# Performance work log

Measured on AMD Instinct MI355X. Metric: run time of the kernel, lower is better.

## Reference

```python
import jax, jax.numpy as jnp
import numpy as np

B, K, M, MN = 256, 32, 64, 256
E, H, Q = 128, 128, 128
NE, NR, NNODES = 100000, 500, 256  # entities, relations, max_nodes


def setup_inputs() -> dict:
    key = jax.random.key(0)
    ks = jax.random.split(key, 24)
    f = lambda k, s: jax.random.normal(k, s, jnp.float32) * 0.05
    inp = {}
    inp['start_entities'] = jax.random.randint(ks[0], (B,), 0, NE)
    inp['aims'] = jax.random.randint(ks[1], (B, K), 0, NE)
    inp['node_pos'] = jnp.broadcast_to(jnp.arange(1, K + 1, dtype=jnp.int32), (B, K))
    inp['neighbor_nodes'] = jax.random.randint(ks[2], (B, K, M), 0, NNODES)
    inp['neighbor_relations'] = jax.random.randint(ks[3], (B, K, M), 0, NR)
    inp['neighbors_num'] = jax.random.randint(ks[4], (B, K), 0, M + 1)
    inp['currents'] = jax.random.randint(ks[5], (B,), 0, NNODES)
    inp['candidate_nodes'] = jax.random.randint(ks[6], (B, MN), 0, NNODES)
    inp['candidate_entities'] = jax.random.randint(ks[7], (B, MN), 0, NE)
    inp['candidate_relations'] = jax.random.randint(ks[8], (B, MN), 0, NR)
    inp['candidate_masks'] = jax.random.randint(ks[9], (B, MN), 0, 2).astype(bool)
    inp['entity_emb'] = f(ks[10], (NE, E))
    inp['relation_emb'] = f(ks[11], (NR, E))
    inp['hidden_W'] = f(ks[12], (H, E)); inp['hidden_b'] = f(ks[13], (H,))
    inp['pass_W'] = f(ks[14], (H, H + E)); inp['pass_b'] = f(ks[15], (H,))
    inp['nexthop_W'] = f(ks[16], (H, H + Q)); inp['nexthop_b'] = f(ks[17], (H,))
    inp['candidate_W'] = f(ks[18], (H, H + 2 * E)); inp['candidate_b'] = f(ks[19], (H,))
    inp['gate_W'] = f(ks[20], (1, H + Q)); inp['gate_b'] = f(ks[21], (1,))
    inp['query'] = f(ks[22], (B, Q))
    return inp


def _linear(x, W, b):
    return x @ W.T + b


def _lrelu(x):
    return jax.nn.leaky_relu(x, 0.01)  # torch LeakyReLU default


def _gather_nodes(node_emb, idx):
    # node_emb: (B, N+2, H), idx: (B, ...) -> (B, ..., H)
    b = node_emb.shape[0]
    g = jnp.take_along_axis(node_emb, idx.reshape(b, -1)[:, :, None], axis=1)
    return g.reshape(*idx.shape, node_emb.shape[-1])


def reference(start_entities, aims, node_pos, neighbor_nodes, neighbor_relations,
              neighbors_num, currents, candidate_nodes, candidate_entities,
              candidate_relations, candidate_masks, entity_emb, relation_emb,
              hidden_W, hidden_b, pass_W, pass_b, nexthop_W, nexthop_b,
              candidate_W, candidate_b, gate_W, gate_b, query):
    # ---- Agent.init ----
    node_emb = jnp.zeros((B, NNODES + 2, H), jnp.float32)
    init = _lrelu(_linear(entity_emb[start_entities], hidden_W, hidden_b))
    node_emb = node_emb.at[:, 0].set(init)
    # ---- Agent.aggregate: gather -> Linear -> masked mean -> scatter ----
    aim_e = entity_emb[aims]                                   # (B,K,E)
    nb_node = _gather_nodes(node_emb, neighbor_nodes)          # (B,K,M,H)
    nb_rel = relation_emb[neighbor_relations]                  # (B,K,M,E)
    nb = _linear(jnp.concatenate([nb_node, nb_rel], -1), pass_W, pass_b)  # pass_activation = identity
    keep = jnp.arange(M) < neighbors_num[:, :, None]           # (B,K,M)
    nb = jnp.where(keep[..., None], nb, 0.0)
    denom = (neighbors_num + (neighbors_num == 0)).astype(jnp.float32)
    agg = nb.sum(axis=2) / denom[..., None]                    # (B,K,H)
    upd = _lrelu(_linear(aim_e, hidden_W, hidden_b) + agg)
    node_emb = node_emb.at[jnp.arange(B)[:, None], node_pos].set(upd)
    # ---- Agent.next_hop ----
    cur = _gather_nodes(node_emb, currents)                    # (B,H)
    cur_cat = jnp.concatenate([cur, query], axis=1)            # (B,H+Q)
    state = _lrelu(_linear(cur_cat, nexthop_W, nexthop_b))     # (B,H)
    cnode = _gather_nodes(node_emb, candidate_nodes)           # (B,MN,H)
    cand = _lrelu(_linear(jnp.concatenate(
        [cnode, entity_emb[candidate_entities], relation_emb[candidate_relations]], -1),
        candidate_W, candidate_b))                             # (B,MN,H)
    thresh = _linear(cur_cat, gate_W, gate_b)                  # (B,1)
    scores = jnp.einsum('bh,bmh->bm', state, cand) / jnp.sqrt(jnp.float32(E))
    scores = jnp.where(candidate_masks, scores, jnp.float32(-100000.0))
    final_scores = jnp.concatenate([scores, thresh], axis=1)   # (B,MN+1)
    return final_scores
```

## Files before the change

### kernel.cpp

```cpp
#include <hip/hip_runtime.h>

#define B 256
#define K 32
#define M 64
#define MN 256
#define E 128
#define H 128
#define Q 128
#define NSLOT 258
#define CTILE 32
#define XPAD 392

typedef __attribute__((ext_vector_type(8))) short short8;
typedef __attribute__((ext_vector_type(4))) short short4b;
typedef __attribute__((ext_vector_type(4))) float f32x4;

__device__ __forceinline__ float lrelu(float x){ return x >= 0.f ? x : 0.01f*x; }

__device__ __forceinline__ unsigned short f2bf(float f){
    unsigned int u = __float_as_uint(f);
    unsigned int r = u + 0x7FFFu + ((u >> 16) & 1u);
    return (unsigned short)(r >> 16);
}

__device__ __forceinline__ short4b pack4(float4 v){
    short4b r;
    r.x = (short)f2bf(v.x); r.y = (short)f2bf(v.y);
    r.z = (short)f2bf(v.z); r.w = (short)f2bf(v.w);
    return r;
}

__device__ __forceinline__ short8 f8_from(const float* __restrict__ p){
    float4 u = *(const float4*)p;
    float4 v = *(const float4*)(p + 4);
    short8 s;
    s[0]=(short)f2bf(u.x); s[1]=(short)f2bf(u.y); s[2]=(short)f2bf(u.z); s[3]=(short)f2bf(u.w);
    s[4]=(short)f2bf(v.x); s[5]=(short)f2bf(v.y); s[6]=(short)f2bf(v.z); s[7]=(short)f2bf(v.w);
    return s;
}

__global__ void k_front(const int* __restrict__ aims, const int* __restrict__ nbr_nodes,
                        const int* __restrict__ nbr_rels, const int* __restrict__ nbr_num,
                        const int* __restrict__ start_ent, const int* __restrict__ node_pos,
                        const float* __restrict__ ent_emb, const float* __restrict__ rel_emb,
                        const float* __restrict__ hW, const float* __restrict__ hb,
                        const float* __restrict__ passW, const float* __restrict__ candW,
                        float* __restrict__ ab, int* __restrict__ map,
                        float* __restrict__ init_out, float* __restrict__ wninit_out,
                        unsigned short* __restrict__ Wf, unsigned short* __restrict__ Wcatf,
                        unsigned short* __restrict__ Pf,
                        unsigned short* __restrict__ XhG, unsigned short* __restrict__ XaG,
                        float* __restrict__ zrow){
    int blk = blockIdx.x, t = threadIdx.x;
    __shared__ float e[128];
    __shared__ float si[128];
    __shared__ unsigned int hist[4][512];
    __shared__ float sden[4];

    if (blk >= 848) {
        int hb4 = blk - 848;
        for (int i = t; i < 2048; i += 256) ((unsigned int*)hist)[i] = 0u;
        __syncthreads();
        int w = t >> 6, lane = t & 63;
        int bk = hb4*4 + w;
        int num = nbr_num[bk];
        int nr  = nbr_rels[(long)bk*M + lane];
        int nn  = nbr_nodes[(long)bk*M + lane];
        unsigned long long mask = __ballot((lane < num) && (nn == 0));
        int c0 = (int)__popcll(mask);
        float denom = (float)(num > 0 ? num : 1);
        if (lane < num) atomicAdd(&hist[w][nr], 1u);
        float2 av = *(const float2*)&ent_emb[(long)aims[bk]*E + lane*2];
        ushort2 ap; ap.x = f2bf(av.x); ap.y = f2bf(av.y);
        *(ushort2*)&XaG[(long)bk*128 + lane*2] = ap;
        if (lane == 0) {
            ab[bk*2+0] = (float)c0 / denom;
            ab[bk*2+1] = (float)num / denom;
            sden[w] = 1.f / denom;
        }
        __syncthreads();
        for (int i = t; i < 2048; i += 256) {
            int w2 = i >> 9, r = i & 511;
            float v = (float)hist[w2][r] * sden[w2];
            XhG[((long)(hb4*4 + w2))*512 + r] = f2bf(v);
        }
        return;
    }

    int pb = blk;
    if (pb < 256) {
        int b = pb;
        if (t < 128) e[t] = ent_emb[(long)start_ent[b]*E + t];
        __syncthreads();
        if (t < 128) {
            float acc = hb[t];
            #pragma unroll 8
            for (int j=0;j<E;j++) acc += hW[t*E+j]*e[j];
            float v = lrelu(acc);
            si[t] = v;
            init_out[b*H+t] = v;
        }
        __syncthreads();
        if (t < 128) {
            float acc2 = 0.f;
            #pragma unroll 8
            for (int j=0;j<H;j++) acc2 += passW[t*(H+E)+j]*si[j];
            wninit_out[b*H+t] = acc2;
        }
    } else if (pb < 512) {
        int b = pb - 256;
        for (int i=t;i<NSLOT;i+=256) map[b*NSLOT+i] = -2;
        __syncthreads();
        if (t==0) map[b*NSLOT+0] = -1;
        __syncthreads();
        if (t<K) map[b*NSLOT + node_pos[b*K+t]] = t;
        if (pb == 256 && t < 128) zrow[t] = 0.f;
    } else if (pb < 704) {
        int i = (pb-512)*256 + t;
        int j = i & 7;
        int l = (i >> 3) & 63;
        int ct = (i >> 9) & 1;
        int r = i >> 10;
        int ks = r % 12, w = r / 12;
        int row = w*32 + ct*16 + (l & 15);
        int col = ks*32 + (l >> 4)*8 + j;
        Wf[i] = f2bf(candW[row*384 + col]);
    } else if (pb < 832) {
        int i = (pb-704)*256 + t;
        int j = i & 7;
        int l = (i >> 3) & 63;
        int ct = (i >> 9) & 1;
        int r = i >> 10;
        int ks = r & 7, w = r >> 3;
        int row = w*32 + ct*16 + (l & 15);
        int col = ks*32 + (l >> 4)*8 + j;
        float v = (col < 128) ? passW[row*256 + 128 + col] : hW[row*128 + (col-128)];
        Wcatf[i] = f2bf(v);
    } else {
        int g = pb - 832;
        int w = t >> 6, lane = t & 63;
        int l16 = lane & 15, lhi = lane >> 4;
        int hbase = w*32;
        const short8 z8 = (short8){0,0,0,0,0,0,0,0};
        f32x4 acc[2][2];
        #pragma unroll
        for (int rt=0;rt<2;rt++)
            #pragma unroll
            for (int ct=0;ct<2;ct++)
                acc[rt][ct] = (f32x4){0.f,0.f,0.f,0.f};
        #pragma unroll
        for (int ks2 = 0; ks2 < 4; ks2++) {
            int kof = ks2*32 + lhi*8;
            int r0 = g*32 + l16, r1 = g*32 + 16 + l16;
            short8 a0 = (r0 < 500) ? f8_from(&rel_emb[(long)r0*E + kof]) : z8;
            short8 a1 = (r1 < 500) ? f8_from(&rel_emb[(long)r1*E + kof]) : z8;
            short8 b0 = f8_from(&passW[(long)(hbase + l16)*(H+E) + H + kof]);
            short8 b1 = f8_from(&passW[(long)(hbase + 16 + l16)*(H+E) + H + kof]);
            acc[0][0] = __builtin_amdgcn_mfma_f32_16x16x32_bf16(a0, b0, acc[0][0], 0, 0, 0);
            acc[0][1] = __builtin_amdgcn_mfma_f32_16x16x32_bf16(a0, b1, acc[0][1], 0, 0, 0);
            acc[1][0] = __builtin_amdgcn_mfma_f32_16x16x32_bf16(a1, b0, acc[1][0], 0, 0, 0);
            acc[1][1] = __builtin_amdgcn_mfma_f32_16x16x32_bf16(a1, b1, acc[1][1], 0, 0, 0);
        }
        #pragma unroll
        for (int rt=0; rt<2; rt++) {
            #pragma unroll
            for (int ct=0; ct<2; ct++) {
                #pragma unroll
                for (int i=0;i<4;i++) {
                    int rp = rt*16 + 4*lhi + i;
                    long idx = ((long)((w*16 + g)*2 + ct))*512 + (l16 + (rp>>3)*16)*8 + (rp & 7);
                    Pf[idx] = f2bf(acc[rt][ct][i]);
                }
            }
        }
    }
}

__global__ void k_updg(const unsigned short* __restrict__ XhG,
                       const unsigned short* __restrict__ XaG,
                       const float* __restrict__ ab,
                       const unsigned short* __restrict__ Wcatf,
                       const unsigned short* __restrict__ Pf,
                       const float* __restrict__ hb_, const float* __restrict__ passb,
                       const float* __restrict__ wninit,
                       const int* __restrict__ currents, const int* __restrict__ map,
                       const float* __restrict__ init, const float* __restrict__ query,
                       const float* __restrict__ nW, const float* __restrict__ nb_,
                       const float* __restrict__ gW, const float* __restrict__ gb,
                       float* __restrict__ upd, float* __restrict__ state,
                       float* __restrict__ out){
    int b = blockIdx.x;
    int t = threadIdx.x;
    __shared__ __align__(16) unsigned short Xh[32][520];
    __shared__ __align__(16) unsigned short Xa[32][136];
    __shared__ float wni[128];
    __shared__ float sab[64];
    __shared__ float cc[H+Q];
    __shared__ float wsum[2];
    #pragma unroll
    for (int it = 0; it < 8; it++) {
        int idx = it*256 + t;
        int r = idx >> 6;
        int cg = (idx & 63) * 8;
        *(short8*)&Xh[r][cg] = *(const short8*)&XhG[((long)b*32 + r)*512 + cg];
    }
    #pragma unroll
    for (int it = 0; it < 2; it++) {
        int idx = it*256 + t;
        int r = idx >> 4;
        int cg = (idx & 15) * 8;
        *(short8*)&Xa[r][cg] = *(const short8*)&XaG[((long)b*32 + r)*128 + cg];
    }
    if (t < 128) wni[t] = wninit[b*128 + t];
    else if (t < 192) sab[t-128] = ab[b*64 + (t-128)];

    int w    = t >> 6;
    int lane = t & 63;
    int l16  = lane & 15;
    int lhi  = lane >> 4;
    int hbase = w*32;
    int mvc = map[b*NSLOT + currents[b]];
    __syncthreads();

    f32x4 acc[2][2];
    #pragma unroll
    for (int rt=0;rt<2;rt++)
        #pragma unroll
        for (int ct=0;ct<2;ct++)
            acc[rt][ct] = (f32x4){0.f,0.f,0.f,0.f};

    #pragma unroll 4
    for (int ks = 0; ks < 16; ks++) {
        int kof = ks*32 + lhi*8;
        short8 a0 = *(const short8*)&Xh[l16][kof];
        short8 a1 = *(const short8*)&Xh[16 + l16][kof];
        short8 b0 = *(const short8*)&Pf[(((long)(w*16+ks)*2 + 0)*64 + lane)*8];
        short8 b1 = *(const short8*)&Pf[(((long)(w*16+ks)*2 + 1)*64 + lane)*8];
        acc[0][0] = __builtin_amdgcn_mfma_f32_16x16x32_bf16(a0, b0, acc[0][0], 0, 0, 0);
        acc[0][1] = __builtin_amdgcn_mfma_f32_16x16x32_bf16(a0, b1, acc[0][1], 0, 0, 0);
        acc[1][0] = __builtin_amdgcn_mfma_f32_16x16x32_bf16(a1, b0, acc[1][0], 0, 0, 0);
        acc[1][1] = __builtin_amdgcn_mfma_f32_16x16x32_bf16(a1, b1, acc[1][1], 0, 0, 0);
    }
    #pragma unroll
    for (int ks2 = 0; ks2 < 4; ks2++) {
        int kof = ks2*32 + lhi*8;
        short8 a0 = *(const short8*)&Xa[l16][kof];
        short8 a1 = *(const short8*)&Xa[16 + l16][kof];
        short8 b0 = *(const short8*)&Wcatf[((((w*8 + 4 + ks2)*2 + 0)*64) + lane)*8];
        short8 b1 = *(const short8*)&Wcatf[((((w*8 + 4 + ks2)*2 + 1)*64) + lane)*8];
        acc[0][0] = __builtin_amdgcn_mfma_f32_16x16x32_bf16(a0, b0, acc[0][0], 0, 0, 0);
        acc[0][1] = __builtin_amdgcn_mfma_f32_16x16x32_bf16(a0, b1, acc[0][1], 0, 0, 0);
        acc[1][0] = __builtin_amdgcn_mfma_f32_16x16x32_bf16(a1, b0, acc[1][0], 0, 0, 0);
        acc[1][1] = __builtin_amdgcn_mfma_f32_16x16x32_bf16(a1, b1, acc[1][1], 0, 0, 0);
    }

    int h0 = hbase + l16, h1 = hbase + 16 + l16;
    float hb0 = hb_[h0], hb1 = hb_[h1];
    float pb0 = passb[h0], pb1 = passb[h1];
    float w0 = wni[h0],  w1 = wni[h1];

    if (t < 128) {
        cc[t] = (mvc == -1) ? init[b*H + t] : 0.f;
        cc[H+t] = query[b*Q + t];
    }

    float uv[2][2][4];
    #pragma unroll
    for (int rt=0; rt<2; rt++) {
        #pragma unroll
        for (int i=0;i<4;i++) {
            int r = rt*16 + 4*lhi + i;
            float al = sab[r*2], be = sab[r*2+1];
            float v0 = lrelu(hb0 + al*w0 + be*pb0 + acc[rt][0][i]);
            float v1 = lrelu(hb1 + al*w1 + be*pb1 + acc[rt][1][i]);
            uv[rt][0][i] = v0; uv[rt][1][i] = v1;
            upd[((long)b*32 + r)*128 + h0] = v0;
            upd[((long)b*32 + r)*128 + h1] = v1;
        }
    }
    __syncthreads();
    if (mvc >= 0) {
        #pragma unroll
        for (int rt=0; rt<2; rt++) {
            #pragma unroll
            for (int i=0;i<4;i++) {
                int r = rt*16 + 4*lhi + i;
                if (r == mvc) { cc[h0] = uv[rt][0][i]; cc[h1] = uv[rt][1][i]; }
            }
        }
    }
    __syncthreads();

    if (t < 128) {
        float sacc = nb_[t];
        #pragma unroll 8
        for (int j=0;j<H+Q;j++) sacc += nW[t*(H+Q)+j]*cc[j];
        state[b*H+t] = lrelu(sacc);
        float tv = gW[t]*cc[t] + gW[H+t]*cc[H+t];
        for (int off=32; off>0; off>>=1) tv += __shfl_down(tv, off);
        if ((t&63)==0) wsum[t>>6] = tv;
    }
    __syncthreads();
    if (t==0) out[b*(MN+1) + MN] = wsum[0] + wsum[1] + gb[0];
}

__global__ void k_cand(const int* __restrict__ cnodes, const int* __restrict__ cents,
                       const int* __restrict__ crels, const int* __restrict__ cmask,
                       const int* __restrict__ map,
                       const float* __restrict__ init, const float* __restrict__ upd,
                       const float* __restrict__ ent_emb, const float* __restrict__ rel_emb,
                       const unsigned short* __restrict__ Wf, const float* __restrict__ cb,
                       const float* __restrict__ state, const float* __restrict__ zrow,
                       float* __restrict__ out){
    int blk = blockIdx.x;
    int b  = blk >> 3;
    int c0 = (blk & 7) * CTILE;
    int t  = threadIdx.x;

    __shared__ __align__(16) unsigned short Xb[CTILE][XPAD];
    __shared__ float sscore[4][CTILE];
    __shared__ int sce[CTILE], scr[CTILE], smv[CTILE];

    if (t < CTILE) {
        int row = b*MN + c0 + t;
        sce[t] = cents[row];
        scr[t] = crels[row];
        smv[t] = map[b*NSLOT + cnodes[row]];
    }
    __syncthreads();

    {
        int c8 = t >> 5;
        int q  = t & 31;
        const float* pn[4]; const float* pe[4]; const float* pr[4];
        #pragma unroll
        for (int i = 0; i < 4; i++) {
            int c = i*8 + c8;
            int mv = smv[c];
            const float* bs = zrow;
            bs = (mv == -1) ? (init + (long)b*H) : bs;
            bs = (mv >= 0)  ? (upd + ((long)b*K + mv)*H) : bs;
            pn[i] = bs + q*4;
            pe[i] = ent_emb + (long)sce[c]*E + q*4;
            pr[i] = rel_emb + (long)scr[c]*E + q*4;
        }
        float4 vn[4], ve[4], vr[4];
        #pragma unroll
        for (int i = 0; i < 4; i++) vn[i] = *(const float4*)pn[i];
        #pragma unroll
        for (int i = 0; i < 4; i++) ve[i] = *(const float4*)pe[i];
        #pragma unroll
        for (int i = 0; i < 4; i++) vr[i] = *(const float4*)pr[i];
        #pragma unroll
        for (int i = 0; i < 4; i++) {
            int cl = i*8 + c8;
            *(short4b*)&Xb[cl][q*4]       = pack4(vn[i]);
            *(short4b*)&Xb[cl][128 + q*4] = pack4(ve[i]);
            *(short4b*)&Xb[cl][256 + q*4] = pack4(vr[i]);
        }
    }

    int w    = t >> 6;
    int lane = t & 63;
    int l16  = lane & 15;
    int lhi  = lane >> 4;

    float s0 = state[b*H + w*32 + l16];
    float s1 = state[b*H + w*32 + 16 + l16];
    float cb0 = cb[w*32 + l16];
    float cb1 = cb[w*32 + 16 + l16];
    __syncthreads();

    f32x4 acc[2][2];
    #pragma unroll
    for (int rt=0;rt<2;rt++)
        #pragma unroll
        for (int ct=0;ct<2;ct++)
            acc[rt][ct] = (f32x4){0.f,0.f,0.f,0.f};

    #pragma unroll
    for (int ks = 0; ks < 12; ks++) {
        int kof = ks*32 + lhi*8;
        short8 b0 = *(const short8*)&Wf[((((w*12+ks)*2+0)*64) + lane)*8];
        short8 b1 = *(const short8*)&Wf[((((w*12+ks)*2+1)*64) + lane)*8];
        short8 a0 = *(const short8*)&Xb[l16][kof];
        short8 a1 = *(const short8*)&Xb[16 + l16][kof];
        acc[0][0] = __builtin_amdgcn_mfma_f32_16x16x32_bf16(a0, b0, acc[0][0], 0, 0, 0);
        acc[0][1] = __builtin_amdgcn_mfma_f32_16x16x32_bf16(a0, b1, acc[0][1], 0, 0, 0);
        acc[1][0] = __builtin_amdgcn_mfma_f32_16x16x32_bf16(a1, b0, acc[1][0], 0, 0, 0);
        acc[1][1] = __builtin_amdgcn_mfma_f32_16x16x32_bf16(a1, b1, acc[1][1], 0, 0, 0);
    }

    #pragma unroll
    for (int rt=0; rt<2; rt++) {
        float ps[4];
        #pragma unroll
        for (int i=0;i<4;i++)
            ps[i] = lrelu(acc[rt][0][i] + cb0)*s0 + lrelu(acc[rt][1][i] + cb1)*s1;
        #pragma unroll
        for (int msk=1; msk<16; msk<<=1) {
            #pragma unroll
            for (int i=0;i<4;i++) ps[i] += __shfl_xor(ps[i], msk);
        }
        if (l16 == 0) {
            #pragma unroll
            for (int i=0;i<4;i++)
                sscore[w][rt*16 + 4*lhi + i] = ps[i];
        }
    }
    __syncthreads();

    if (t < CTILE) {
        int row = b*MN + c0 + t;
        float s = (sscore[0][t] + sscore[1][t] + sscore[2][t] + sscore[3][t])
                  * 0.08838834764831845f;
        out[b*(MN+1) + c0 + t] = cmask[row] ? s : -100000.0f;
    }
}

extern "C" void kernel_launch(void* const* d_in, const int* in_sizes, int n_in,
                              void* d_out, int out_size, void* d_ws, size_t ws_size,
                              hipStream_t stream){
    (void)in_sizes; (void)n_in; (void)out_size; (void)ws_size;
    const int* start_entities      = (const int*)d_in[0];
    const int* aims                = (const int*)d_in[1];
    const int* node_pos            = (const int*)d_in[2];
    const int* neighbor_nodes      = (const int*)d_in[3];
    const int* neighbor_relations  = (const int*)d_in[4];
    const int* neighbors_num       = (const int*)d_in[5];
    const int* currents            = (const int*)d_in[6];
    const int* candidate_nodes     = (const int*)d_in[7];
    const int* candidate_entities  = (const int*)d_in[8];
    const int* candidate_relations = (const int*)d_in[9];
    const int* candidate_masks     = (const int*)d_in[10];
    const float* entity_emb   = (const float*)d_in[11];
    const float* relation_emb = (const float*)d_in[12];
    const float* hidden_W     = (const float*)d_in[13];
    const float* hidden_b     = (const float*)d_in[14];
    const float* pass_W       = (const float*)d_in[15];
    const float* pass_b       = (const float*)d_in[16];
    const float* nexthop_W    = (const float*)d_in[17];
    const float* nexthop_b    = (const float*)d_in[18];
    const float* candidate_W  = (const float*)d_in[19];
    const float* candidate_b  = (const float*)d_in[20];
    const float* gate_W       = (const float*)d_in[21];
    const float* gate_b       = (const float*)d_in[22];
    const float* query        = (const float*)d_in[23];
    float* out = (float*)d_out;

    float* ws     = (float*)d_ws;
    float* init   = ws;
    float* wninit = init + B*H;
    float* upd    = wninit + B*H;
    float* state  = upd + (long)B*K*H;
    float* ab     = state + B*H;
    float* zrow   = ab + B*K*2;
    int*   map    = (int*)(zrow + 128);
    unsigned short* Wf    = (unsigned short*)(map + B*NSLOT);
    unsigned short* Wcatf = Wf + 49152;
    unsigned short* Pf    = Wcatf + 32768;
    unsigned short* XhG   = Pf + 65536;
    unsigned short* XaG   = XhG + (long)B*K*512;

    k_front<<<848 + (B*K)/4, 256, 0, stream>>>(aims, neighbor_nodes, neighbor_relations,
                                               neighbors_num, start_entities, node_pos,
                                               entity_emb, relation_emb,
                                               hidden_W, hidden_b, pass_W, candidate_W,
                                               ab, map, init, wninit, Wf, Wcatf,
                                               Pf, XhG, XaG, zrow);
    k_updg<<<B, 256, 0, stream>>>(XhG, XaG, ab, Wcatf, Pf, hidden_b, pass_b, wninit,
                                  currents, map, init, query,
                                  nexthop_W, nexthop_b, gate_W, gate_b,
                                  upd, state, out);
    k_cand<<<B*(MN/CTILE), 256, 0, stream>>>(candidate_nodes, candidate_entities,
                                             candidate_relations, candidate_masks,
                                             map, init, upd, entity_emb, relation_emb,
                                             Wf, candidate_b, state, zrow, out);
}
```

Measured before the change: 50.23 us.

## Restructure candidate kernel to per-wave 32x32 MFMA tiles without LDS staging

The candidate scoring kernel now gives each wave a whole 32-candidate tile and computes all 128 hidden outputs with 32x32x16 bf16 MFMAs. The A operand is loaded straight from global embeddings into registers, with no LDS staging or block barriers. The candidate weight pre-pack in the front kernel is rearranged to match the new fragment layout. Each wave now reads the whole weight matrix instead of a quarter of it, and register pressure rises with four 16-wide accumulators. In exchange, LDS traffic, synchronisation and the cross-wave score reduction are removed.

```diff
diff --git a/kernel.cpp b/kernel.cpp
--- a/kernel.cpp
+++ b/kernel.cpp
@@ -8,12 +8,10 @@
 #define H 128
 #define Q 128
 #define NSLOT 258
-#define CTILE 32
-#define XPAD 392
 
 typedef __attribute__((ext_vector_type(8))) short short8;
-typedef __attribute__((ext_vector_type(4))) short short4b;
 typedef __attribute__((ext_vector_type(4))) float f32x4;
+typedef __attribute__((ext_vector_type(16))) float f32x16;
 
 __device__ __forceinline__ float lrelu(float x){ return x >= 0.f ? x : 0.01f*x; }
 
@@ -21,13 +19,6 @@
     unsigned int u = __float_as_uint(f);
     unsigned int r = u + 0x7FFFu + ((u >> 16) & 1u);
     return (unsigned short)(r >> 16);
-}
-
-__device__ __forceinline__ short4b pack4(float4 v){
-    short4b r;
-    r.x = (short)f2bf(v.x); r.y = (short)f2bf(v.y);
-    r.z = (short)f2bf(v.z); r.w = (short)f2bf(v.w);
-    return r;
 }
 
 __device__ __forceinline__ short8 f8_from(const float* __restrict__ p){
@@ -47,7 +38,7 @@
                         const float* __restrict__ passW, const float* __restrict__ candW,
                         float* __restrict__ ab, int* __restrict__ map,
                         float* __restrict__ init_out, float* __restrict__ wninit_out,
-                        unsigned short* __restrict__ Wf, unsigned short* __restrict__ Wcatf,
+                        unsigned short* __restrict__ Wf32, unsigned short* __restrict__ Wcatf,
                         unsigned short* __restrict__ Pf,
                         unsigned short* __restrict__ XhG, unsigned short* __restrict__ XaG,
                         float* __restrict__ zrow){
@@ -119,12 +110,11 @@
         int i = (pb-512)*256 + t;
         int j = i & 7;
         int l = (i >> 3) & 63;
-        int ct = (i >> 9) & 1;
-        int r = i >> 10;
-        int ks = r % 12, w = r / 12;
-        int row = w*32 + ct*16 + (l & 15);
-        int col = ks*32 + (l >> 4)*8 + j;
-        Wf[i] = f2bf(candW[row*384 + col]);
+        int r = i >> 9;
+        int s = r % 24, ct = r / 24;
+        int row = ct*32 + (l & 31);
+        int col = s*16 + (l >> 5)*8 + j;
+        Wf32[i] = f2bf(candW[row*384 + col]);
     } else if (pb < 832) {
         int i = (pb-704)*256 + t;
         int j = i & 7;
@@ -304,117 +294,79 @@
     if (t==0) out[b*(MN+1) + MN] = wsum[0] + wsum[1] + gb[0];
 }
 
-__global__ void k_cand(const int* __restrict__ cnodes, const int* __restrict__ cents,
-                       const int* __restrict__ crels, const int* __restrict__ cmask,
-                       const int* __restrict__ map,
-                       const float* __restrict__ init, const float* __restrict__ upd,
-                       const float* __restrict__ ent_emb, const float* __restrict__ rel_emb,
-                       const unsigned short* __restrict__ Wf, const float* __restrict__ cb,
-                       const float* __restrict__ state, const float* __restrict__ zrow,
-                       float* __restrict__ out){
+__global__ __launch_bounds__(256, 3)
+void k_cand(const int* __restrict__ cnodes, const int* __restrict__ cents,
+            const int* __restrict__ crels, const int* __restrict__ cmask,
+            const int* __restrict__ map,
+            const float* __restrict__ init, const float* __restrict__ upd,
+            const float* __restrict__ ent_emb, const float* __restrict__ rel_emb,
+            const unsigned short* __restrict__ Wf32, const float* __restrict__ cb,
+            const float* __restrict__ state, const float* __restrict__ zrow,
+            float* __restrict__ out){
     int blk = blockIdx.x;
-    int b  = blk >> 3;
-    int c0 = (blk & 7) * CTILE;
-    int t  = threadIdx.x;
-
-    __shared__ __align__(16) unsigned short Xb[CTILE][XPAD];
-    __shared__ float sscore[4][CTILE];
-    __shared__ int sce[CTILE], scr[CTILE], smv[CTILE];
-
-    if (t < CTILE) {
-        int row = b*MN + c0 + t;
-        sce[t] = cents[row];
-        scr[t] = crels[row];
-        smv[t] = map[b*NSLOT + cnodes[row]];
-    }
-    __syncthreads();
-
-    {
-        int c8 = t >> 5;
-        int q  = t & 31;
-        const float* pn[4]; const float* pe[4]; const float* pr[4];
-        #pragma unroll
-        for (int i = 0; i < 4; i++) {
-            int c = i*8 + c8;
-            int mv = smv[c];
-            const float* bs = zrow;
-            bs = (mv == -1) ? (init + (long)b*H) : bs;
-            bs = (mv >= 0)  ? (upd + ((long)b*K + mv)*H) : bs;
-            pn[i] = bs + q*4;
-            pe[i] = ent_emb + (long)sce[c]*E + q*4;
-            pr[i] = rel_emb + (long)scr[c]*E + q*4;
-        }
-        float4 vn[4], ve[4], vr[4];
-        #pragma unroll
-        for (int i = 0; i < 4; i++) vn[i] = *(const float4*)pn[i];
-        #pragma unroll
-        for (int i = 0; i < 4; i++) ve[i] = *(const float4*)pe[i];
-        #pragma unroll
-        for (int i = 0; i < 4; i++) vr[i] = *(const float4*)pr[i];
-        #pragma unroll
-        for (int i = 0; i < 4; i++) {
-            int cl = i*8 + c8;
-            *(short4b*)&Xb[cl][q*4]       = pack4(vn[i]);
-            *(short4b*)&Xb[cl][128 + q*4] = pack4(ve[i]);
-            *(short4b*)&Xb[cl][256 + q*4] = pack4(vr[i]);
-        }
-    }
-
-    int w    = t >> 6;
-    int lane = t & 63;
-    int l16  = lane & 15;
-    int lhi  = lane >> 4;
-
-    float s0 = state[b*H + w*32 + l16];
-    float s1 = state[b*H + w*32 + 16 + l16];
-    float cb0 = cb[w*32 + l16];
-    float cb1 = cb[w*32 + 16 + l16];
-    __syncthreads();
-
-    f32x4 acc[2][2];
-    #pragma unroll
-    for (int rt=0;rt<2;rt++)
-        #pragma unroll
-        for (int ct=0;ct<2;ct++)
-            acc[rt][ct] = (f32x4){0.f,0.f,0.f,0.f};
-
-    #pragma unroll
-    for (int ks = 0; ks < 12; ks++) {
-        int kof = ks*32 + lhi*8;
-        short8 b0 = *(const short8*)&Wf[((((w*12+ks)*2+0)*64) + lane)*8];
-        short8 b1 = *(const short8*)&Wf[((((w*12+ks)*2+1)*64) + lane)*8];
-        short8 a0 = *(const short8*)&Xb[l16][kof];
-        short8 a1 = *(const short8*)&Xb[16 + l16][kof];
-        acc[0][0] = __builtin_amdgcn_mfma_f32_16x16x32_bf16(a0, b0, acc[0][0], 0, 0, 0);
-        acc[0][1] = __builtin_amdgcn_mfma_f32_16x16x32_bf16(a0, b1, acc[0][1], 0, 0, 0);
-        acc[1][0] = __builtin_amdgcn_mfma_f32_16x16x32_bf16(a1, b0, acc[1][0], 0, 0, 0);
-        acc[1][1] = __builtin_amdgcn_mfma_f32_16x16x32_bf16(a1, b1, acc[1][1], 0, 0, 0);
-    }
-
-    #pragma unroll
-    for (int rt=0; rt<2; rt++) {
-        float ps[4];
-        #pragma unroll
-        for (int i=0;i<4;i++)
-            ps[i] = lrelu(acc[rt][0][i] + cb0)*s0 + lrelu(acc[rt][1][i] + cb1)*s1;
-        #pragma unroll
-        for (int msk=1; msk<16; msk<<=1) {
-            #pragma unroll
-            for (int i=0;i<4;i++) ps[i] += __shfl_xor(ps[i], msk);
-        }
-        if (l16 == 0) {
-            #pragma unroll
-            for (int i=0;i<4;i++)
-                sscore[w][rt*16 + 4*lhi + i] = ps[i];
-        }
-    }
-    __syncthreads();
-
-    if (t < CTILE) {
-        int row = b*MN + c0 + t;
-        float s = (sscore[0][t] + sscore[1][t] + sscore[2][t] + sscore[3][t])
-                  * 0.08838834764831845f;
-        out[b*(MN+1) + c0 + t] = cmask[row] ? s : -100000.0f;
+    int t = threadIdx.x;
+    int w = t >> 6, lane = t & 63;
+    int tile = blk*4 + w;
+    int b  = tile >> 3;
+    int c0 = (tile & 7) * 32;
+    int l32 = lane & 31;
+    int kh  = (lane >> 5) * 8;
+
+    int row = b*MN + c0 + l32;
+    int cn = cnodes[row];
+    int ce = cents[row];
+    int cr = crels[row];
+    int mv = map[b*NSLOT + cn];
+    const float* pn = zrow;
+    pn = (mv == -1) ? (init + (long)b*H) : pn;
+    pn = (mv >= 0)  ? (upd + ((long)b*K + mv)*H) : pn;
+    const float* pe = ent_emb + (long)ce*E;
+    const float* pr = rel_emb + (long)cr*E;
+
+    f32x16 acc[4];
+    #pragma unroll
+    for (int ct=0; ct<4; ct++)
+        #pragma unroll
+        for (int i=0;i<16;i++) acc[ct][i] = 0.f;
+
+    #pragma unroll
+    for (int s = 0; s < 24; s++) {
+        const float* src = (s < 8)  ? (pn + s*16 + kh)
+                         : (s < 16) ? (pe + (s-8)*16 + kh)
+                                    : (pr + (s-16)*16 + kh);
+        short8 a = f8_from(src);
+        #pragma unroll
+        for (int ct = 0; ct < 4; ct++) {
+            short8 bfr = *(const short8*)&Wf32[(((long)(ct*24 + s)*64) + lane)*8];
+            acc[ct] = __builtin_amdgcn_mfma_f32_32x32x16_bf16(a, bfr, acc[ct], 0, 0, 0);
+        }
+    }
+
+    float ps[16];
+    #pragma unroll
+    for (int r=0;r<16;r++) ps[r] = 0.f;
+    #pragma unroll
+    for (int ct=0; ct<4; ct++) {
+        float st  = state[b*H + ct*32 + l32];
+        float cbv = cb[ct*32 + l32];
+        #pragma unroll
+        for (int r=0;r<16;r++)
+            ps[r] += lrelu(acc[ct][r] + cbv) * st;
+    }
+    #pragma unroll
+    for (int msk=1; msk<32; msk<<=1) {
+        #pragma unroll
+        for (int r=0;r<16;r++) ps[r] += __shfl_xor(ps[r], msk);
+    }
+    if (l32 == 0) {
+        int hi4 = (lane >> 5) * 4;
+        #pragma unroll
+        for (int r=0;r<16;r++) {
+            int crow = (r & 3) + 8*(r >> 2) + hi4;
+            int orow = b*MN + c0 + crow;
+            float s = ps[r] * 0.08838834764831845f;
+            out[b*(MN+1) + c0 + crow] = cmask[orow] ? s : -100000.0f;
+        }
     }
 }
 
@@ -456,8 +408,8 @@
     float* ab     = state + B*H;
     float* zrow   = ab + B*K*2;
     int*   map    = (int*)(zrow + 128);
-    unsigned short* Wf    = (unsigned short*)(map + B*NSLOT);
-    unsigned short* Wcatf = Wf + 49152;
+    unsigned short* Wf32  = (unsigned short*)(map + B*NSLOT);
+    unsigned short* Wcatf = Wf32 + 49152;
     unsigned short* Pf    = Wcatf + 32768;
     unsigned short* XhG   = Pf + 65536;
     unsigned short* XaG   = XhG + (long)B*K*512;
@@ -466,14 +418,14 @@
                                                neighbors_num, start_entities, node_pos,
                                                entity_emb, relation_emb,
                                                hidden_W, hidden_b, pass_W, candidate_W,
-                                               ab, map, init, wninit, Wf, Wcatf,
+                                               ab, map, init, wninit, Wf32, Wcatf,
                                                Pf, XhG, XaG, zrow);
     k_updg<<<B, 256, 0, stream>>>(XhG, XaG, ab, Wcatf, Pf, hidden_b, pass_b, wninit,
                                   currents, map, init, query,
                                   nexthop_W, nexthop_b, gate_W, gate_b,
                                   upd, state, out);
-    k_cand<<<B*(MN/CTILE), 256, 0, stream>>>(candidate_nodes, candidate_entities,
-                                             candidate_relations, candidate_masks,
-                                             map, init, upd, entity_emb, relation_emb,
-                                             Wf, candidate_b, state, zrow, out);
-}
+    k_cand<<<(B*(MN/32))/4, 256, 0, stream>>>(candidate_nodes, candidate_entities,
+                                              candidate_relations, candidate_masks,
+                                              map, init, upd, entity_emb, relation_emb,
+                                              Wf32, candidate_b, state, zrow, out);
+}
```

Result: slower. 54.56 us (+8.6%).
